# Kernel tuning notes

Hardware: AMD Instinct MI355X
Metric: run time of the kernel (lower is better)

## Reference

```python
import jax, jax.numpy as jnp
import numpy as np

N = 50000   # nodes
F = 128     # num_features (per branch)
E = 800000  # edges
G = 16      # graphs in batch
T = 3       # blocks per branch


def setup_inputs() -> dict:
    key = jax.random.key(0)
    ks = jax.random.split(key, 32)
    s = 0.05
    d = {}
    d["x"] = jax.random.normal(ks[0], (N, 2 * F), jnp.float32)
    d["edge_index"] = jax.random.randint(ks[1], (2, E), 0, N)
    d["edge_weight"] = jax.random.uniform(ks[2], (E,), jnp.float32)
    d["batch"] = jnp.sort(jax.random.randint(ks[3], (N,), 0, G))
    d["states"] = jax.random.randint(ks[4], (N,), 0, 2).astype(jnp.float32)

    def w(k, shape):
        return jax.random.normal(k, shape, jnp.float32) * s

    for i, p in enumerate(["p1", "p2"]):
        b = 5 + i * 5
        d[f"{p}_a0"] = w(ks[b], (T,))            # alpha0: Linear(1,1,bias=False) weight per block
        d[f"{p}_a1W"] = w(ks[b + 1], (T, F, F))    # alpha1 weight
        d[f"{p}_a1b"] = w(ks[b + 2], (T, F))       # alpha1 bias
        d[f"{p}_linW"] = w(ks[b + 3], (T, F, F))   # conv.lin weight
        d[f"{p}_linb"] = w(ks[b + 4], (T, F))      # conv.lin bias
    d["beta0_W"] = w(ks[15], (F, F))
    d["beta1_W"] = w(ks[16], (F, F))
    d["beta2_W"] = w(ks[17], (F, 2 * F))
    d["beta2_b"] = w(ks[18], (F,))
    d["gamma0_W"] = w(ks[19], (F, F))
    d["gamma1_W"] = w(ks[20], (F, F))
    d["gamma2_W"] = w(ks[21], (F, F))
    d["gamma3_W"] = w(ks[22], (3 * F // 2, 3 * F))
    d["gamma4_W"] = w(ks[23], (1, 3 * F // 2))
    d["gamma4_b"] = w(ks[24], (1,))
    return d


def _lrelu(v):
    return jax.nn.leaky_relu(v, 0.2)


def _block(x, states, a0, a1W, a1b, linW, linb, src, dst, ew):
    # x = lrelu(alpha1(x + alpha0(states)))
    h = _lrelu((x + states[:, None] * a0) @ a1W.T + a1b)
    # CustomGCNConv: lin then edge-weighted gather/scatter-add (source->target)
    h = h @ linW.T + linb
    msg = ew[:, None] * h[src]  # [E, F]
    return jax.ops.segment_sum(msg, dst, num_segments=x.shape[0])


def reference(x, edge_index, edge_weight, batch, states,
              p1_a0, p1_a1W, p1_a1b, p1_linW, p1_linb,
              p2_a0, p2_a1W, p2_a1b, p2_linW, p2_linb,
              beta0_W, beta1_W, beta2_W, beta2_b,
              gamma0_W, gamma1_W, gamma2_W, gamma3_W, gamma4_W, gamma4_b):
    Fh = x.shape[1] // 2
    x1, x2 = x[:, :Fh], x[:, Fh:]
    s0, s1 = edge_index[0], edge_index[1]
    x1s = jnp.zeros_like(x1)
    x2s = jnp.zeros_like(x2)
    for t in range(T):
        # branch1 uses reversed edges edge_index[[1,0]]
        x1 = _lrelu(_block(x1, states, p1_a0[t], p1_a1W[t], p1_a1b[t],
                           p1_linW[t], p1_linb[t], s1, s0, edge_weight))
        x2 = _lrelu(_block(x2, states, p2_a0[t], p2_a1W[t], p2_a1b[t],
                           p2_linW[t], p2_linb[t], s0, s1, edge_weight))
        x1s = x1s + x1
        x2s = x2s + x2
    xc = _lrelu(jnp.concatenate([x1s @ beta0_W.T, x2s @ beta1_W.T], -1) @ beta2_W.T + beta2_b)
    sel = (states == 1.0)[:, None]
    # per-graph pooled sums broadcast back to nodes (== repeat_interleave since batch is sorted)
    x_s = jax.ops.segment_sum(jnp.where(sel, xc, 0.0), batch, num_segments=G)[batch]
    x_sum = jax.ops.segment_sum(xc, batch, num_segments=G)[batch]
    h = jnp.concatenate([xc @ gamma0_W.T, x_s @ gamma1_W.T, x_sum @ gamma2_W.T], -1)
    h = _lrelu(h @ gamma3_W.T)
    return (h @ gamma4_W.T + gamma4_b).reshape(-1)
```

## Files before the change

### kernel.cpp

```cpp
#include <hip/hip_runtime.h>

typedef short s8v __attribute__((ext_vector_type(8)));
typedef float f32x4 __attribute__((ext_vector_type(4)));

#define LRELU(v) ((v) > 0.f ? (v) : 0.2f * (v))

constexpr int NBK = 391;
constexpr int TILE = 2048;
constexpr int CAP = 4096;

__device__ __forceinline__ float b2f(unsigned short b) {
  return __uint_as_float(((unsigned int)b) << 16);
}
__device__ __forceinline__ unsigned short f2b(float f) {
  unsigned int x = __float_as_uint(f);
  x += 0x7fffu + ((x >> 16) & 1u);
  return (unsigned short)(x >> 16);
}
__device__ __forceinline__ unsigned int pack2(float lo, float hi) {
  return ((unsigned int)f2b(hi) << 16) | (unsigned int)f2b(lo);
}

struct FArgs {
  const unsigned short* X[2];
  const unsigned short* W1[2];
  const float* b1[2];
  const float* a0p[2];
  const float* rowsum[2];
  const unsigned short* W2[2];
  const float* b2[2];
  unsigned short* H[2];
  const float* states;
  int N;
};

__global__ __launch_bounds__(256) void fused_mlp_kernel(FArgs fa)
{
  __shared__ __align__(16) unsigned short Ws[128 * 128];
  __shared__ __align__(16) unsigned short Tp[128 * 128];
  const int d = blockIdx.y;
  const int tid = threadIdx.x;
  const int lane = tid & 63;
  const int w = tid >> 6;
  const int l15 = lane & 15;
  const int g = lane >> 4;
  const int m0 = blockIdx.x * 128;
  const int N = fa.N;

#pragma unroll
  for (int j = 0; j < 8; ++j) {
    int idx = tid + j * 256;
    int o = idx >> 4, c = idx & 15;
    uint4 v = *(const uint4*)(fa.W1[d] + (size_t)o * 128 + c * 8);
    *(uint4*)&Ws[o * 128 + (c ^ (o & 15)) * 8] = v;
  }
  s8v a[2][4];
#pragma unroll
  for (int mf = 0; mf < 2; ++mf) {
    int row = m0 + w * 32 + mf * 16 + l15;
    const unsigned short* ar = fa.X[d] + (size_t)row * 128 + g * 8;
#pragma unroll
    for (int ks = 0; ks < 4; ++ks) {
      s8v t = {};
      if (row < N) t = *(const s8v*)(ar + ks * 32);
      a[mf][ks] = t;
    }
  }
  f32x4 zero4 = {0.f, 0.f, 0.f, 0.f};
  f32x4 acc[2][8];
#pragma unroll
  for (int mf = 0; mf < 2; ++mf)
#pragma unroll
    for (int nf = 0; nf < 8; ++nf) acc[mf][nf] = zero4;
  __syncthreads();
#pragma unroll
  for (int ks = 0; ks < 4; ++ks) {
#pragma unroll
    for (int nf = 0; nf < 8; ++nf) {
      int c = ks * 4 + g;
      s8v b = *(const s8v*)&Ws[(nf * 16 + l15) * 128 + (c ^ l15) * 8];
      acc[0][nf] = __builtin_amdgcn_mfma_f32_16x16x32_bf16(a[0][ks], b, acc[0][nf], 0, 0, 0);
      acc[1][nf] = __builtin_amdgcn_mfma_f32_16x16x32_bf16(a[1][ks], b, acc[1][nf], 0, 0, 0);
    }
  }
  const float a0 = fa.a0p[d][0];
#pragma unroll
  for (int mf = 0; mf < 2; ++mf) {
#pragma unroll
    for (int r = 0; r < 4; ++r) {
      int lrow = w * 32 + mf * 16 + g * 4 + r;
      int row = m0 + lrow;
      float sa = (row < N) ? fa.states[row] * a0 : 0.f;
#pragma unroll
      for (int nf = 0; nf < 8; ++nf) {
        int col = nf * 16 + l15;
        float v = 0.f;
        if (row < N) {
          v = acc[mf][nf][r] + fa.b1[d][col] + sa * fa.rowsum[d][col];
          v = LRELU(v);
        }
        int cch = col >> 3;
        Tp[lrow * 128 + ((cch ^ (lrow & 15)) << 3) + (col & 7)] = f2b(v);
      }
    }
  }
  __syncthreads();
#pragma unroll
  for (int j = 0; j < 8; ++j) {
    int idx = tid + j * 256;
    int o = idx >> 4, c = idx & 15;
    uint4 v = *(const uint4*)(fa.W2[d] + (size_t)o * 128 + c * 8);
    *(uint4*)&Ws[o * 128 + (c ^ (o & 15)) * 8] = v;
  }
  __syncthreads();
#pragma unroll
  for (int mf = 0; mf < 2; ++mf) {
    int lrow = w * 32 + mf * 16 + l15;
#pragma unroll
    for (int ks = 0; ks < 4; ++ks) {
      int c2 = ks * 4 + g;
      a[mf][ks] = *(const s8v*)&Tp[lrow * 128 + ((c2 ^ (lrow & 15)) << 3)];
    }
  }
#pragma unroll
  for (int mf = 0; mf < 2; ++mf)
#pragma unroll
    for (int nf = 0; nf < 8; ++nf) acc[mf][nf] = zero4;
#pragma unroll
  for (int ks = 0; ks < 4; ++ks) {
#pragma unroll
    for (int nf = 0; nf < 8; ++nf) {
      int c = ks * 4 + g;
      s8v b = *(const s8v*)&Ws[(nf * 16 + l15) * 128 + (c ^ l15) * 8];
      acc[0][nf] = __builtin_amdgcn_mfma_f32_16x16x32_bf16(a[0][ks], b, acc[0][nf], 0, 0, 0);
      acc[1][nf] = __builtin_amdgcn_mfma_f32_16x16x32_bf16(a[1][ks], b, acc[1][nf], 0, 0, 0);
    }
  }
#pragma unroll
  for (int mf = 0; mf < 2; ++mf) {
#pragma unroll
    for (int r = 0; r < 4; ++r) {
      int row = m0 + w * 32 + mf * 16 + g * 4 + r;
      if (row >= N) continue;
      unsigned short* crow = fa.H[d] + (size_t)row * 128;
#pragma unroll
      for (int nf = 0; nf < 8; ++nf) {
        int col = nf * 16 + l15;
        crow[col] = f2b(acc[mf][nf][r] + fa.b2[d][col]);
      }
    }
  }
}

struct PBArgs {
  const unsigned short* U[2];
  const unsigned short* Wb[2];
  const unsigned short* Wb2;
  const float* bias;
  unsigned short* XC;
  int N;
};

__global__ __launch_bounds__(256) void fused_beta_kernel(PBArgs pa)
{
  __shared__ __align__(16) unsigned short Ws[128 * 128];
  __shared__ __align__(16) unsigned short Tp[128 * 128];
  const int tid = threadIdx.x;
  const int lane = tid & 63;
  const int w = tid >> 6;
  const int l15 = lane & 15;
  const int g = lane >> 4;
  const int m0 = blockIdx.x * 128;
  const int N = pa.N;
  f32x4 zero4 = {0.f, 0.f, 0.f, 0.f};
  s8v a[2][4];
  f32x4 accf[2][8];
#pragma unroll
  for (int mf = 0; mf < 2; ++mf)
#pragma unroll
    for (int nf = 0; nf < 8; ++nf) accf[mf][nf] = zero4;

  for (int ph = 0; ph < 2; ++ph) {
#pragma unroll
    for (int j = 0; j < 8; ++j) {
      int idx = tid + j * 256;
      int o = idx >> 4, c = idx & 15;
      uint4 v = *(const uint4*)(pa.Wb[ph] + (size_t)o * 128 + c * 8);
      *(uint4*)&Ws[o * 128 + (c ^ (o & 15)) * 8] = v;
    }
#pragma unroll
    for (int mf = 0; mf < 2; ++mf) {
      int row = m0 + w * 32 + mf * 16 + l15;
      const unsigned short* ar = pa.U[ph] + (size_t)row * 128 + g * 8;
#pragma unroll
      for (int ks = 0; ks < 4; ++ks) {
        s8v t = {};
        if (row < N) t = *(const s8v*)(ar + ks * 32);
        a[mf][ks] = t;
      }
    }
    f32x4 acc[2][8];
#pragma unroll
    for (int mf = 0; mf < 2; ++mf)
#pragma unroll
      for (int nf = 0; nf < 8; ++nf) acc[mf][nf] = zero4;
    __syncthreads();
#pragma unroll
    for (int ks = 0; ks < 4; ++ks) {
#pragma unroll
      for (int nf = 0; nf < 8; ++nf) {
        int c = ks * 4 + g;
        s8v b = *(const s8v*)&Ws[(nf * 16 + l15) * 128 + (c ^ l15) * 8];
        acc[0][nf] = __builtin_amdgcn_mfma_f32_16x16x32_bf16(a[0][ks], b, acc[0][nf], 0, 0, 0);
        acc[1][nf] = __builtin_amdgcn_mfma_f32_16x16x32_bf16(a[1][ks], b, acc[1][nf], 0, 0, 0);
      }
    }
    __syncthreads();
#pragma unroll
    for (int mf = 0; mf < 2; ++mf) {
#pragma unroll
      for (int r = 0; r < 4; ++r) {
        int lrow = w * 32 + mf * 16 + g * 4 + r;
        int row = m0 + lrow;
#pragma unroll
        for (int nf = 0; nf < 8; ++nf) {
          int col = nf * 16 + l15;
          float v = (row < N) ? acc[mf][nf][r] : 0.f;
          int cch = col >> 3;
          Tp[lrow * 128 + ((cch ^ (lrow & 15)) << 3) + (col & 7)] = f2b(v);
        }
      }
    }
    __syncthreads();
#pragma unroll
    for (int j = 0; j < 8; ++j) {
      int idx = tid + j * 256;
      int o = idx >> 4, c = idx & 15;
      uint4 v = *(const uint4*)(pa.Wb2 + (size_t)o * 256 + ph * 128 + c * 8);
      *(uint4*)&Ws[o * 128 + (c ^ (o & 15)) * 8] = v;
    }
#pragma unroll
    for (int mf = 0; mf < 2; ++mf) {
      int lrow = w * 32 + mf * 16 + l15;
#pragma unroll
      for (int ks = 0; ks < 4; ++ks) {
        int c2 = ks * 4 + g;
        a[mf][ks] = *(const s8v*)&Tp[lrow * 128 + ((c2 ^ (lrow & 15)) << 3)];
      }
    }
    __syncthreads();
#pragma unroll
    for (int ks = 0; ks < 4; ++ks) {
#pragma unroll
      for (int nf = 0; nf < 8; ++nf) {
        int c = ks * 4 + g;
        s8v b = *(const s8v*)&Ws[(nf * 16 + l15) * 128 + (c ^ l15) * 8];
        accf[0][nf] = __builtin_amdgcn_mfma_f32_16x16x32_bf16(a[0][ks], b, accf[0][nf], 0, 0, 0);
        accf[1][nf] = __builtin_amdgcn_mfma_f32_16x16x32_bf16(a[1][ks], b, accf[1][nf], 0, 0, 0);
      }
    }
    __syncthreads();
  }
#pragma unroll
  for (int mf = 0; mf < 2; ++mf) {
#pragma unroll
    for (int r = 0; r < 4; ++r) {
      int row = m0 + w * 32 + mf * 16 + g * 4 + r;
      if (row >= N) continue;
      unsigned short* crow = pa.XC + (size_t)row * 128;
#pragma unroll
      for (int nf = 0; nf < 8; ++nf) {
        int col = nf * 16 + l15;
        float v = accf[mf][nf][r] + pa.bias[col];
        crow[col] = f2b(LRELU(v));
      }
    }
  }
}

__global__ __launch_bounds__(256) void g3_kernel(
    const unsigned short* __restrict__ xc,
    const unsigned short* __restrict__ A16,
    const unsigned short* __restrict__ B16,
    const int* __restrict__ batch,
    const unsigned short* __restrict__ W0,
    const unsigned short* __restrict__ W3,
    const float* __restrict__ g4W,
    const float* __restrict__ g4b,
    float* __restrict__ out, int N)
{
  constexpr int NF = 12;
  __shared__ __align__(16) unsigned short Ws[192 * 128];
  __shared__ __align__(16) unsigned short Tp[128 * 128];
  const int tid = threadIdx.x;
  const int lane = tid & 63;
  const int w = tid >> 6;
  const int l15 = lane & 15;
  const int g = lane >> 4;
  const int m0 = blockIdx.x * 128;

  f32x4 zero4 = {0.f, 0.f, 0.f, 0.f};
  s8v a[2][4];

#pragma unroll
  for (int j = 0; j < 8; ++j) {
    int idx = tid + j * 256;
    int o = idx >> 4, c = idx & 15;
    uint4 v = *(const uint4*)(W0 + (size_t)o * 128 + c * 8);
    *(uint4*)&Ws[o * 128 + (c ^ (o & 15)) * 8] = v;
  }
#pragma unroll
  for (int mf = 0; mf < 2; ++mf) {
    int row = m0 + w * 32 + mf * 16 + l15;
    const unsigned short* ar = xc + (size_t)row * 128 + g * 8;
#pragma unroll
    for (int ks = 0; ks < 4; ++ks) {
      s8v t = {};
      if (row < N) t = *(const s8v*)(ar + ks * 32);
      a[mf][ks] = t;
    }
  }
  {
    f32x4 acc1[2][8];
#pragma unroll
    for (int mf = 0; mf < 2; ++mf)
#pragma unroll
      for (int nf = 0; nf < 8; ++nf) acc1[mf][nf] = zero4;
    __syncthreads();
#pragma unroll
    for (int ks = 0; ks < 4; ++ks) {
#pragma unroll
      for (int nf = 0; nf < 8; ++nf) {
        int c = ks * 4 + g;
        s8v b = *(const s8v*)&Ws[(nf * 16 + l15) * 128 + (c ^ l15) * 8];
        acc1[0][nf] = __builtin_amdgcn_mfma_f32_16x16x32_bf16(a[0][ks], b, acc1[0][nf], 0, 0, 0);
        acc1[1][nf] = __builtin_amdgcn_mfma_f32_16x16x32_bf16(a[1][ks], b, acc1[1][nf], 0, 0, 0);
      }
    }
#pragma unroll
    for (int mf = 0; mf < 2; ++mf) {
#pragma unroll
      for (int r = 0; r < 4; ++r) {
        int lrow = w * 32 + mf * 16 + g * 4 + r;
        int row = m0 + lrow;
#pragma unroll
        for (int nf = 0; nf < 8; ++nf) {
          int col = nf * 16 + l15;
          float v = (row < N) ? acc1[mf][nf][r] : 0.f;
          int cch = col >> 3;
          Tp[lrow * 128 + ((cch ^ (lrow & 15)) << 3) + (col & 7)] = f2b(v);
        }
      }
    }
  }
  __syncthreads();

  f32x4 acc[2][NF];
#pragma unroll
  for (int mf = 0; mf < 2; ++mf)
#pragma unroll
    for (int nf = 0; nf < NF; ++nf) acc[mf][nf] = zero4;

  int brow[2];
#pragma unroll
  for (int mf = 0; mf < 2; ++mf) {
    int row = m0 + w * 32 + mf * 16 + l15;
    brow[mf] = (row < N) ? batch[row] : 0;
  }

  for (int kk = 0; kk < 384; kk += 128) {
#pragma unroll
    for (int j = 0; j < NF; ++j) {
      int idx = tid + j * 256;
      int o = idx >> 4, c = idx & 15;
      uint4 v = *(const uint4*)(W3 + (size_t)o * 384 + kk + c * 8);
      *(uint4*)&Ws[o * 128 + (c ^ (o & 15)) * 8] = v;
    }
    if (kk == 0) {
#pragma unroll
      for (int mf = 0; mf < 2; ++mf) {
        int lrow = w * 32 + mf * 16 + l15;
#pragma unroll
        for (int ks = 0; ks < 4; ++ks) {
          int c2 = ks * 4 + g;
          a[mf][ks] = *(const s8v*)&Tp[lrow * 128 + ((c2 ^ (lrow & 15)) << 3)];
        }
      }
    } else {
#pragma unroll
      for (int mf = 0; mf < 2; ++mf) {
        int row = m0 + w * 32 + mf * 16 + l15;
        const unsigned short* ar = ((kk == 128) ? A16 : B16) + (size_t)brow[mf] * 128 + g * 8;
#pragma unroll
        for (int ks = 0; ks < 4; ++ks) {
          s8v t = {};
          if (row < N) t = *(const s8v*)(ar + ks * 32);
          a[mf][ks] = t;
        }
      }
    }
    __syncthreads();
#pragma unroll
    for (int ks = 0; ks < 4; ++ks) {
#pragma unroll
      for (int nf = 0; nf < NF; ++nf) {
        int c = ks * 4 + g;
        s8v b = *(const s8v*)&Ws[(nf * 16 + l15) * 128 + (c ^ l15) * 8];
        acc[0][nf] = __builtin_amdgcn_mfma_f32_16x16x32_bf16(a[0][ks], b, acc[0][nf], 0, 0, 0);
        acc[1][nf] = __builtin_amdgcn_mfma_f32_16x16x32_bf16(a[1][ks], b, acc[1][nf], 0, 0, 0);
      }
    }
    if (kk < 256) __syncthreads();
  }

  float w4[NF];
#pragma unroll
  for (int nf = 0; nf < NF; ++nf) w4[nf] = g4W[nf * 16 + l15];
  const float gb = g4b[0];

#pragma unroll
  for (int mf = 0; mf < 2; ++mf) {
#pragma unroll
    for (int r = 0; r < 4; ++r) {
      int row = m0 + w * 32 + mf * 16 + g * 4 + r;
      float dot = 0.f;
#pragma unroll
      for (int nf = 0; nf < NF; ++nf) {
        float v = acc[mf][nf][r];
        v = LRELU(v);
        dot += v * w4[nf];
      }
#pragma unroll
      for (int m = 1; m < 16; m <<= 1) dot += __shfl_xor(dot, m, 16);
      if (l15 == 0 && row < N) out[row] = dot + gb;
    }
  }
}

struct PreArgs {
  const float* src[9];
  unsigned short* wreg;
  int cum[10];
  const float* a1; const float* a2; float* rs;
  const float* x;
  unsigned short* x1; unsigned short* x2;
  int* bcur0; int* bcur1;
  int n;
};

__global__ __launch_bounds__(256) void preamble_kernel(PreArgs pa)
{
  const int NINIT = 3125;
  const int NCONV = 172;
  int b = blockIdx.x;
  int t = threadIdx.x;
  if (b < NINIT) {
    int idx = b * 256 + t;
    if (idx < pa.n * 16) {
      int r = idx >> 4, c = idx & 15;
      const float* xr = pa.x + (size_t)r * 256 + c * 8;
      float4 p0 = *(const float4*)xr;
      float4 p1 = *(const float4*)(xr + 4);
      uint4 u1;
      u1.x = pack2(p0.x, p0.y); u1.y = pack2(p0.z, p0.w);
      u1.z = pack2(p1.x, p1.y); u1.w = pack2(p1.z, p1.w);
      float4 q0 = *(const float4*)(xr + 128);
      float4 q1 = *(const float4*)(xr + 132);
      uint4 u2;
      u2.x = pack2(q0.x, q0.y); u2.y = pack2(q0.z, q0.w);
      u2.z = pack2(q1.x, q1.y); u2.w = pack2(q1.z, q1.w);
      ((uint4*)(pa.x1 + (size_t)r * 128))[c] = u1;
      ((uint4*)(pa.x2 + (size_t)r * 128))[c] = u2;
    }
  } else if (b < NINIT + NCONV) {
    int e = ((b - NINIT) * 256 + t) * 8;
    if (e < pa.cum[9]) {
      int j = 0;
#pragma unroll
      for (int k = 1; k < 9; ++k) if (e >= pa.cum[k]) j = k;
      const float* s = pa.src[j] + (e - pa.cum[j]);
      float4 p0 = *(const float4*)s;
      float4 p1 = *(const float4*)(s + 4);
      uint4 u;
      u.x = pack2(p0.x, p0.y); u.y = pack2(p0.z, p0.w);
      u.z = pack2(p1.x, p1.y); u.w = pack2(p1.z, p1.w);
      *(uint4*)(pa.wreg + e) = u;
    }
  } else if (b < NINIT + NCONV + 6) {
    int j = b - NINIT - NCONV;
    if (t < 128) {
      const float* src = (j < 3) ? (pa.a1 + (size_t)j * 16384) : (pa.a2 + (size_t)(j - 3) * 16384);
      float s = 0.f;
      for (int k = 0; k < 128; ++k) s += src[t * 128 + k];
      pa.rs[j * 128 + t] = s;
    }
  } else {
    for (int i = t; i < NBK; i += 256) { pa.bcur0[i] = 0; pa.bcur1[i] = 0; }
  }
}

struct BinArgs {
  const int* s0; const int* s1; const float* ew;
  int* bcur0; int* bcur1;
  unsigned long long* bin0; unsigned long long* bin1;
  int E;
};
__global__ __launch_bounds__(256) void bin_kernel(BinArgs ba)
{
  __shared__ int hist0[NBK], hist1[NBK];
  __shared__ int base0[NBK], base1[NBK];
  const int t = threadIdx.x;
  const int e0 = blockIdx.x * TILE;
  const int e1 = min(e0 + TILE, ba.E);
  for (int i = t; i < NBK; i += 256) { hist0[i] = 0; hist1[i] = 0; }
  __syncthreads();
  for (int e = e0 + t; e < e1; e += 256) {
    atomicAdd(&hist0[ba.s0[e] >> 7], 1);
    atomicAdd(&hist1[ba.s1[e] >> 7], 1);
  }
  __syncthreads();
  for (int i = t; i < NBK; i += 256) {
    int c0 = hist0[i];
    base0[i] = c0 ? atomicAdd(&ba.bcur0[i], c0) : 0;
    int c1 = hist1[i];
    base1[i] = c1 ? atomicAdd(&ba.bcur1[i], c1) : 0;
  }
  __syncthreads();
  for (int i = t; i < NBK; i += 256) { hist0[i] = 0; hist1[i] = 0; }
  __syncthreads();
  for (int e = e0 + t; e < e1; e += 256) {
    int d0 = ba.s0[e], d1 = ba.s1[e];
    unsigned long long wb = (unsigned long long)__float_as_uint(ba.ew[e]) << 32;
    int b0 = d0 >> 7, b1 = d1 >> 7;
    int r0 = base0[b0] + atomicAdd(&hist0[b0], 1);
    if (r0 < CAP)
      ba.bin0[(size_t)b0 * CAP + r0] = wb | (unsigned int)((d0 & 127) << 16) | (unsigned int)d1;
    int r1 = base1[b1] + atomicAdd(&hist1[b1], 1);
    if (r1 < CAP)
      ba.bin1[(size_t)b1 * CAP + r1] = wb | (unsigned int)((d1 & 127) << 16) | (unsigned int)d0;
  }
}

struct BScanArgs { const int* cnt[2]; int* bbase[2]; float* gsel; float* gsum; };
__global__ __launch_bounds__(128) void bscan_kernel(BScanArgs a)
{
  __shared__ int ld[2][NBK];
  int wid = threadIdx.x >> 6, lane = threadIdx.x & 63;
  for (int i = threadIdx.x; i < 2048; i += 128) { a.gsel[i] = 0.f; a.gsum[i] = 0.f; }
  for (int i = lane; i < NBK; i += 64) ld[wid][i] = a.cnt[wid][i];
  __syncthreads();
  if (lane == 0) {
    int acc = 0;
    for (int i = 0; i < NBK; ++i) { int v = ld[wid][i]; ld[wid][i] = acc; acc += v; }
    a.bbase[wid][NBK] = acc;
  }
  __syncthreads();
  for (int i = lane; i < NBK; i += 64) a.bbase[wid][i] = ld[wid][i];
}

struct RArgs {
  const int* bbase[2];
  const unsigned long long* bin[2];
  unsigned int* comb[2];
  int* row[2];
  int n;
};
__global__ __launch_bounds__(256) void reorder_kernel(RArgs ra)
{
  const int d = blockIdx.y;
  const int b = blockIdx.x;
  const unsigned long long* __restrict__ bin = ra.bin[d] + (size_t)b * CAP;
  unsigned int* __restrict__ comb = ra.comb[d];
  int* __restrict__ row = ra.row[d];
  const int nb = b * 128;
  const int ne = min(nb + 128, ra.n);
  const int t = threadIdx.x;
  __shared__ int lcnt[128];
  __shared__ int lcur[128];
  __shared__ int wtot[4];
  if (t < 128) lcnt[t] = 0;
  const int span_beg = ra.bbase[d][b];
  const int span_end = ra.bbase[d][b + 1];
  const int cnt = span_end - span_beg;
  __syncthreads();
  for (int i = t; i < cnt; i += 256) {
    int nl = ((unsigned int)bin[i] >> 16) & 127;
    atomicAdd(&lcnt[nl], 1);
  }
  __syncthreads();
  int lane = t & 63, wv = t >> 6;
  int v = (t < 128) ? lcnt[t] : 0;
  int sc = v;
#pragma unroll
  for (int off = 1; off < 64; off <<= 1) {
    int u = __shfl_up(sc, off, 64);
    if (lane >= off) sc += u;
  }
  if (lane == 63) wtot[wv] = sc;
  __syncthreads();
  int excl = sc - v + ((wv == 1) ? wtot[0] : 0);
  if (t < 128) {
    lcur[t] = excl;
    if (nb + t < ne) row[nb + t] = span_beg + excl;
  }
  if (b == NBK - 1 && t == 0) row[ra.n] = span_end;
  __syncthreads();
  for (int i = t; i < cnt; i += 256) {
    unsigned long long r = bin[i];
    unsigned int lo = (unsigned int)r;
    float w = __uint_as_float((unsigned int)(r >> 32));
    int nl = (lo >> 16) & 127;
    int slot = atomicAdd(&lcur[nl], 1);
    comb[span_beg + slot] = (lo & 0xffffu) | ((unsigned int)f2b(w) << 16);
  }
}

struct GArgs {
  const int* rowstart[2];
  const unsigned int* comb[2];
  const unsigned short* h[2];
  unsigned short* xout[2];
  const unsigned int* add1[2];
  const unsigned int* add2[2];
  int n;
};
__global__ void gather_kernel(GArgs ga)
{
  int quad = blockIdx.x * (blockDim.x >> 6) + (threadIdx.x >> 6);
  int lane = threadIdx.x & 63;
  int sub = lane >> 4;
  int fl = lane & 15;
  long long gnode = (long long)4 * quad + sub;
  bool valid = gnode < 2 * ga.n;
  int dir = (valid && gnode >= ga.n) ? 1 : 0;
  int node = valid ? (int)(gnode - (long long)dir * ga.n) : 0;
  const int* __restrict__ rowstart = ga.rowstart[dir];
  const unsigned int* __restrict__ comb = ga.comb[dir];
  const unsigned int* __restrict__ h = (const unsigned int*)ga.h[dir];
  int beg = rowstart[node], end = rowstart[node + 1];
  if (!valid) end = beg;
  int nch_own = (end - beg + 7) >> 3;
  int m1 = max(nch_own, __shfl_xor(nch_own, 16, 64));
  int nch = max(m1, __shfl_xor(m1, 32, 64));
  float a0 = 0.f, a1 = 0.f, a2 = 0.f, a3 = 0.f;
  float a4 = 0.f, a5 = 0.f, a6 = 0.f, a7 = 0.f;
  for (int ch = 0; ch < nch; ++ch) {
    int p0 = beg + ch * 8;
    unsigned int cc[8];
    uint4 uu[8];
#pragma unroll
    for (int i = 0; i < 8; ++i) {
      int pi = p0 + i;
      cc[i] = (pi < end) ? comb[pi] : 0u;
    }
#pragma unroll
    for (int i = 0; i < 8; ++i)
      uu[i] = *(const uint4*)(h + (size_t)(cc[i] & 0xffffu) * 64 + fl * 4);
#pragma unroll
    for (int i = 0; i < 8; ++i) {
      float wv = b2f((unsigned short)(cc[i] >> 16));
      a0 += wv * b2f((unsigned short)uu[i].x);
      a1 += wv * b2f((unsigned short)(uu[i].x >> 16));
      a2 += wv * b2f((unsigned short)uu[i].y);
      a3 += wv * b2f((unsigned short)(uu[i].y >> 16));
      a4 += wv * b2f((unsigned short)uu[i].z);
      a5 += wv * b2f((unsigned short)(uu[i].z >> 16));
      a6 += wv * b2f((unsigned short)uu[i].w);
      a7 += wv * b2f((unsigned short)(uu[i].w >> 16));
    }
  }
  float v0 = LRELU(a0), v1 = LRELU(a1), v2 = LRELU(a2), v3 = LRELU(a3);
  float v4 = LRELU(a4), v5 = LRELU(a5), v6 = LRELU(a6), v7 = LRELU(a7);
  if (ga.add1[0]) {
    uint4 ua = ((const uint4*)ga.add1[dir])[(size_t)node * 16 + fl];
    uint4 ub = ((const uint4*)ga.add2[dir])[(size_t)node * 16 + fl];
    v0 += b2f((unsigned short)ua.x) + b2f((unsigned short)ub.x);
    v1 += b2f((unsigned short)(ua.x >> 16)) + b2f((unsigned short)(ub.x >> 16));
    v2 += b2f((unsigned short)ua.y) + b2f((unsigned short)ub.y);
    v3 += b2f((unsigned short)(ua.y >> 16)) + b2f((unsigned short)(ub.y >> 16));
    v4 += b2f((unsigned short)ua.z) + b2f((unsigned short)ub.z);
    v5 += b2f((unsigned short)(ua.z >> 16)) + b2f((unsigned short)(ub.z >> 16));
    v6 += b2f((unsigned short)ua.w) + b2f((unsigned short)ub.w);
    v7 += b2f((unsigned short)(ua.w >> 16)) + b2f((unsigned short)(ub.w >> 16));
  }
  if (valid) {
    uint4 o;
    o.x = pack2(v0, v1);
    o.y = pack2(v2, v3);
    o.z = pack2(v4, v5);
    o.w = pack2(v6, v7);
    ((uint4*)(ga.xout[dir] + (size_t)node * 128))[fl] = o;
  }
}

__global__ __launch_bounds__(256) void segsum_kernel(
    const unsigned short* __restrict__ xc, const int* __restrict__ batch,
    const float* __restrict__ states,
    float* __restrict__ gsel, float* __restrict__ gsum, int n)
{
  int slot = threadIdx.x >> 6;
  int lane = threadIdx.x & 63;
  int r0 = blockIdx.x * 128 + slot * 32;
  if (r0 >= n) return;
  int r1 = min(r0 + 32, n);
  const unsigned int* __restrict__ xcu = (const unsigned int*)xc;
  float sel0 = 0.f, sel1 = 0.f, sum0 = 0.f, sum1 = 0.f;
  int cur = batch[r0];
  for (int r = r0; r < r1; r += 4) {
    unsigned int u[4]; int bb[4]; float st[4];
#pragma unroll
    for (int i = 0; i < 4; ++i) {
      int ri = min(r + i, r1 - 1);
      u[i] = xcu[(size_t)ri * 64 + lane];
      bb[i] = batch[ri];
      st[i] = states[ri];
    }
    int m = min(4, r1 - r);
#pragma unroll
    for (int i = 0; i < 4; ++i) {
      if (i >= m) break;
      if (bb[i] != cur) {
        atomicAdd(&gsel[cur * 128 + lane * 2], sel0);
        atomicAdd(&gsel[cur * 128 + lane * 2 + 1], sel1);
        atomicAdd(&gsum[cur * 128 + lane * 2], sum0);
        atomicAdd(&gsum[cur * 128 + lane * 2 + 1], sum1);
        sel0 = sel1 = sum0 = sum1 = 0.f;
        cur = bb[i];
      }
      float lo = b2f((unsigned short)u[i]);
      float hi = b2f((unsigned short)(u[i] >> 16));
      sum0 += lo; sum1 += hi;
      if (st[i] == 1.0f) { sel0 += lo; sel1 += hi; }
    }
  }
  atomicAdd(&gsel[cur * 128 + lane * 2], sel0);
  atomicAdd(&gsel[cur * 128 + lane * 2 + 1], sel1);
  atomicAdd(&gsum[cur * 128 + lane * 2], sum0);
  atomicAdd(&gsum[cur * 128 + lane * 2 + 1], sum1);
}

__global__ void small16_kernel(const float* __restrict__ gsel, const float* __restrict__ gsum,
                               const float* __restrict__ g1W, const float* __restrict__ g2W,
                               unsigned short* __restrict__ A16, unsigned short* __restrict__ B16)
{
  int r = blockIdx.x, t = threadIdx.x, o = t & 127;
  const float* src = (t < 128) ? gsel : gsum;
  const float* Wm  = (t < 128) ? g1W : g2W;
  float acc = 0.f;
  for (int k = 0; k < 128; ++k) acc += src[r * 128 + k] * Wm[o * 128 + k];
  unsigned short* dst = (t < 128) ? A16 : B16;
  dst[r * 128 + o] = f2b(acc);
}

extern "C" void kernel_launch(void* const* d_in, const int* in_sizes, int n_in,
                              void* d_out, int out_size, void* d_ws, size_t ws_size,
                              hipStream_t stream)
{
  const int N = 50000, F = 128, E = 800000, G = 16, T = 3;
  const float* x      = (const float*)d_in[0];
  const int*   ei     = (const int*)d_in[1];
  const int*   s0     = ei;
  const int*   s1     = ei + E;
  const float* ew     = (const float*)d_in[2];
  const int*   batch  = (const int*)d_in[3];
  const float* states = (const float*)d_in[4];
  const float* p_a0[2]   = {(const float*)d_in[5],  (const float*)d_in[10]};
  const float* p_a1W[2]  = {(const float*)d_in[6],  (const float*)d_in[11]};
  const float* p_a1b[2]  = {(const float*)d_in[7],  (const float*)d_in[12]};
  const float* p_linW[2] = {(const float*)d_in[8],  (const float*)d_in[13]};
  const float* p_linb[2] = {(const float*)d_in[9],  (const float*)d_in[14]};
  const float* beta0W = (const float*)d_in[15];
  const float* beta1W = (const float*)d_in[16];
  const float* beta2W = (const float*)d_in[17];
  const float* beta2b = (const float*)d_in[18];
  const float* g0W = (const float*)d_in[19];
  const float* g1W = (const float*)d_in[20];
  const float* g2W = (const float*)d_in[21];
  const float* g3W = (const float*)d_in[22];
  const float* g4W = (const float*)d_in[23];
  const float* g4b = (const float*)d_in[24];
  float* out = (float*)d_out;

  char* p = (char*)d_ws;
  auto alloc = [&](size_t bytes) {
    char* r = p;
    p += (bytes + 255) & ~(size_t)255;
    return r;
  };
  const size_t NFb2 = (size_t)N * F * sizeof(unsigned short);
  unsigned short* X1[3] = {(unsigned short*)alloc(NFb2), (unsigned short*)alloc(NFb2),
                           (unsigned short*)alloc(NFb2)};
  unsigned short* X2[3] = {(unsigned short*)alloc(NFb2), (unsigned short*)alloc(NFb2),
                           (unsigned short*)alloc(NFb2)};
  unsigned short* TMP0 = (unsigned short*)alloc(NFb2);
  unsigned short* TMP1 = (unsigned short*)alloc(NFb2);
  unsigned short* HH0  = (unsigned short*)alloc(NFb2);
  unsigned short* HH1  = (unsigned short*)alloc(NFb2);
  int*   row0 = (int*)alloc((size_t)(N + 1) * 4);
  int*   row1 = (int*)alloc((size_t)(N + 1) * 4);
  int*   bbase0 = (int*)alloc((size_t)(NBK + 1) * 4);
  int*   bbase1 = (int*)alloc((size_t)(NBK + 1) * 4);
  int*   bcur0 = (int*)alloc((size_t)NBK * 4);
  int*   bcur1 = (int*)alloc((size_t)NBK * 4);
  unsigned long long* bin0 = (unsigned long long*)alloc((size_t)NBK * CAP * 8);
  unsigned long long* bin1 = (unsigned long long*)alloc((size_t)NBK * CAP * 8);
  unsigned int* comb0 = (unsigned int*)alloc((size_t)E * 4);
  unsigned int* comb1 = (unsigned int*)alloc((size_t)E * 4);
  float* gsel = (float*)alloc((size_t)G * F * 4);
  float* gsum = (float*)alloc((size_t)G * F * 4);
  unsigned short* A16b = (unsigned short*)alloc((size_t)G * F * 2);
  unsigned short* B16b = (unsigned short*)alloc((size_t)G * F * 2);
  unsigned short* wreg = (unsigned short*)alloc((size_t)352256 * 2);
  float* rs = (float*)alloc((size_t)6 * 128 * 4);

  unsigned short* a1Wb[2]  = {wreg + 0,      wreg + 49152};
  unsigned short* linWb[2] = {wreg + 98304,  wreg + 147456};
  unsigned short* b0b = wreg + 196608;
  unsigned short* b1b = wreg + 212992;
  unsigned short* b2b = wreg + 229376;
  unsigned short* g0b = wreg + 262144;
  unsigned short* g3b = wreg + 278528;

  const dim3 blk256(256);
  const int GX = (N + 127) / 128;
  const int EB = (E + TILE - 1) / TILE;

  PreArgs pra;
  pra.src[0] = p_a1W[0];  pra.src[1] = p_a1W[1];
  pra.src[2] = p_linW[0]; pra.src[3] = p_linW[1];
  pra.src[4] = beta0W;    pra.src[5] = beta1W;  pra.src[6] = beta2W;
  pra.src[7] = g0W;       pra.src[8] = g3W;
  pra.wreg = wreg;
  int cums[10] = {0, 49152, 98304, 147456, 196608, 212992, 229376, 262144, 278528, 352256};
  for (int i = 0; i < 10; ++i) pra.cum[i] = cums[i];
  pra.a1 = p_a1W[0]; pra.a2 = p_a1W[1]; pra.rs = rs;
  pra.x = x; pra.x1 = X1[0]; pra.x2 = X2[0];
  pra.bcur0 = bcur0; pra.bcur1 = bcur1;
  pra.n = N;
  preamble_kernel<<<3125 + 172 + 6 + 1, blk256, 0, stream>>>(pra);

  BinArgs bna;
  bna.s0 = s0; bna.s1 = s1; bna.ew = ew;
  bna.bcur0 = bcur0; bna.bcur1 = bcur1;
  bna.bin0 = bin0; bna.bin1 = bin1;
  bna.E = E;
  bin_kernel<<<EB, blk256, 0, stream>>>(bna);
  BScanArgs bsa;
  bsa.cnt[0] = bcur0; bsa.cnt[1] = bcur1;
  bsa.bbase[0] = bbase0; bsa.bbase[1] = bbase1;
  bsa.gsel = gsel; bsa.gsum = gsum;
  bscan_kernel<<<1, 128, 0, stream>>>(bsa);
  RArgs ra;
  ra.bbase[0] = bbase0; ra.bbase[1] = bbase1;
  ra.bin[0] = bin0; ra.bin[1] = bin1;
  ra.comb[0] = comb0; ra.comb[1] = comb1;
  ra.row[0] = row0; ra.row[1] = row1;
  ra.n = N;
  reorder_kernel<<<dim3(NBK, 2), blk256, 0, stream>>>(ra);

  for (int t = 0; t < T; ++t) {
    int rv = t % 3, wv = (t + 1) % 3;

    FArgs fa;
    fa.X[0] = X1[rv];  fa.X[1] = X2[rv];
    fa.W1[0] = a1Wb[0] + t * 16384;  fa.W1[1] = a1Wb[1] + t * 16384;
    fa.b1[0] = p_a1b[0] + t * F;     fa.b1[1] = p_a1b[1] + t * F;
    fa.a0p[0] = p_a0[0] + t;         fa.a0p[1] = p_a0[1] + t;
    fa.rowsum[0] = rs + t * 128;     fa.rowsum[1] = rs + (3 + t) * 128;
    fa.W2[0] = linWb[0] + t * 16384; fa.W2[1] = linWb[1] + t * 16384;
    fa.b2[0] = p_linb[0] + t * F;    fa.b2[1] = p_linb[1] + t * F;
    fa.H[0] = HH0;  fa.H[1] = HH1;
    fa.states = states;  fa.N = N;
    fused_mlp_kernel<<<dim3(GX, 2), blk256, 0, stream>>>(fa);

    GArgs ga;
    ga.rowstart[0] = row0; ga.rowstart[1] = row1;
    ga.comb[0] = comb0;    ga.comb[1] = comb1;
    ga.h[0] = HH0;         ga.h[1] = HH1;
    if (t == T - 1) {
      ga.xout[0] = TMP0;  ga.xout[1] = TMP1;
      ga.add1[0] = (const unsigned int*)X1[1];  ga.add1[1] = (const unsigned int*)X2[1];
      ga.add2[0] = (const unsigned int*)X1[2];  ga.add2[1] = (const unsigned int*)X2[2];
    } else {
      ga.xout[0] = X1[wv];  ga.xout[1] = X2[wv];
      ga.add1[0] = nullptr; ga.add1[1] = nullptr;
      ga.add2[0] = nullptr; ga.add2[1] = nullptr;
    }
    ga.n = N;
    gather_kernel<<<(2 * N + 15) / 16, blk256, 0, stream>>>(ga);
  }

  PBArgs pb;
  pb.U[0] = TMP0; pb.U[1] = TMP1;
  pb.Wb[0] = b0b; pb.Wb[1] = b1b; pb.Wb2 = b2b;
  pb.bias = beta2b; pb.XC = HH0; pb.N = N;
  fused_beta_kernel<<<GX, blk256, 0, stream>>>(pb);

  segsum_kernel<<<GX, blk256, 0, stream>>>(HH0, batch, states, gsel, gsum, N);
  small16_kernel<<<G, blk256, 0, stream>>>(gsel, gsum, g1W, g2W, A16b, B16b);

  g3_kernel<<<GX, blk256, 0, stream>>>(HH0, A16b, B16b, batch, g0b, g3b, g4W, g4b, out, N);
}
```

Before: 406.1 us.

## Sort gather nodes by degree to balance wavefront loop trip counts

Builds a per-direction degree histogram during reordering, then a new kernel produces a permutation grouping nodes by in-degree (capped at 63). The gather kernel processes nodes in this permuted order, so the four nodes sharing a wavefront have similar chunk counts and less divergence from the max-reduced loop bound. This adds a small kernel, atomics and an extra indirection, and scatters the output writes and row reads across memory.

```diff
diff --git a/kernel.cpp b/kernel.cpp
--- a/kernel.cpp
+++ b/kernel.cpp
@@ -541,12 +541,14 @@
   }
 }
 
-struct BScanArgs { const int* cnt[2]; int* bbase[2]; float* gsel; float* gsum; };
+struct BScanArgs { const int* cnt[2]; int* bbase[2]; float* gsel; float* gsum;
+                   int* dhist; int* dcur; };
 __global__ __launch_bounds__(128) void bscan_kernel(BScanArgs a)
 {
   __shared__ int ld[2][NBK];
   int wid = threadIdx.x >> 6, lane = threadIdx.x & 63;
   for (int i = threadIdx.x; i < 2048; i += 128) { a.gsel[i] = 0.f; a.gsum[i] = 0.f; }
+  if (threadIdx.x < 128) { a.dhist[threadIdx.x] = 0; a.dcur[threadIdx.x] = 0; }
   for (int i = lane; i < NBK; i += 64) ld[wid][i] = a.cnt[wid][i];
   __syncthreads();
   if (lane == 0) {
@@ -563,6 +565,7 @@
   const unsigned long long* bin[2];
   unsigned int* comb[2];
   int* row[2];
+  int* dhist;
   int n;
 };
 __global__ __launch_bounds__(256) void reorder_kernel(RArgs ra)
@@ -590,6 +593,7 @@
   __syncthreads();
   int lane = t & 63, wv = t >> 6;
   int v = (t < 128) ? lcnt[t] : 0;
+  if (t < 128 && nb + t < ne) atomicAdd(&ra.dhist[d * 64 + min(v, 63)], 1);
   int sc = v;
 #pragma unroll
   for (int off = 1; off < 64; off <<= 1) {
@@ -615,6 +619,31 @@
   }
 }
 
+struct DPArgs {
+  const int* row[2];
+  const int* dhist;
+  int* dcur;
+  int* perm[2];
+  int n;
+};
+__global__ __launch_bounds__(256) void dperm_kernel(DPArgs a)
+{
+  const int d = blockIdx.y;
+  const int i = blockIdx.x * 256 + threadIdx.x;
+  __shared__ int sbase[64];
+  if (threadIdx.x == 0) {
+    int acc = 0;
+    for (int k = 0; k < 64; ++k) { sbase[k] = acc; acc += a.dhist[d * 64 + k]; }
+  }
+  __syncthreads();
+  if (i < a.n) {
+    int deg = a.row[d][i + 1] - a.row[d][i];
+    int bin = min(deg, 63);
+    int pos = sbase[bin] + atomicAdd(&a.dcur[d * 64 + bin], 1);
+    a.perm[d][pos] = i;
+  }
+}
+
 struct GArgs {
   const int* rowstart[2];
   const unsigned int* comb[2];
@@ -622,6 +651,7 @@
   unsigned short* xout[2];
   const unsigned int* add1[2];
   const unsigned int* add2[2];
+  const int* perm[2];
   int n;
 };
 __global__ void gather_kernel(GArgs ga)
@@ -633,7 +663,8 @@
   long long gnode = (long long)4 * quad + sub;
   bool valid = gnode < 2 * ga.n;
   int dir = (valid && gnode >= ga.n) ? 1 : 0;
-  int node = valid ? (int)(gnode - (long long)dir * ga.n) : 0;
+  int pidx = valid ? (int)(gnode - (long long)dir * ga.n) : 0;
+  int node = ga.perm[dir][pidx];
   const int* __restrict__ rowstart = ga.rowstart[dir];
   const unsigned int* __restrict__ comb = ga.comb[dir];
   const unsigned int* __restrict__ h = (const unsigned int*)ga.h[dir];
@@ -806,6 +837,10 @@
   unsigned long long* bin1 = (unsigned long long*)alloc((size_t)NBK * CAP * 8);
   unsigned int* comb0 = (unsigned int*)alloc((size_t)E * 4);
   unsigned int* comb1 = (unsigned int*)alloc((size_t)E * 4);
+  int*   perm0 = (int*)alloc((size_t)N * 4);
+  int*   perm1 = (int*)alloc((size_t)N * 4);
+  int*   dhist = (int*)alloc((size_t)128 * 4);
+  int*   dcur  = (int*)alloc((size_t)128 * 4);
   float* gsel = (float*)alloc((size_t)G * F * 4);
   float* gsum = (float*)alloc((size_t)G * F * 4);
   unsigned short* A16b = (unsigned short*)alloc((size_t)G * F * 2);
@@ -849,14 +884,22 @@
   bsa.cnt[0] = bcur0; bsa.cnt[1] = bcur1;
   bsa.bbase[0] = bbase0; bsa.bbase[1] = bbase1;
   bsa.gsel = gsel; bsa.gsum = gsum;
+  bsa.dhist = dhist; bsa.dcur = dcur;
   bscan_kernel<<<1, 128, 0, stream>>>(bsa);
   RArgs ra;
   ra.bbase[0] = bbase0; ra.bbase[1] = bbase1;
   ra.bin[0] = bin0; ra.bin[1] = bin1;
   ra.comb[0] = comb0; ra.comb[1] = comb1;
   ra.row[0] = row0; ra.row[1] = row1;
+  ra.dhist = dhist;
   ra.n = N;
   reorder_kernel<<<dim3(NBK, 2), blk256, 0, stream>>>(ra);
+  DPArgs dpa;
+  dpa.row[0] = row0; dpa.row[1] = row1;
+  dpa.dhist = dhist; dpa.dcur = dcur;
+  dpa.perm[0] = perm0; dpa.perm[1] = perm1;
+  dpa.n = N;
+  dperm_kernel<<<dim3((N + 255) / 256, 2), blk256, 0, stream>>>(dpa);
 
   for (int t = 0; t < T; ++t) {
     int rv = t % 3, wv = (t + 1) % 3;
@@ -877,6 +920,7 @@
     ga.rowstart[0] = row0; ga.rowstart[1] = row1;
     ga.comb[0] = comb0;    ga.comb[1] = comb1;
     ga.h[0] = HH0;         ga.h[1] = HH1;
+    ga.perm[0] = perm0;    ga.perm[1] = perm1;
     if (t == T - 1) {
       ga.xout[0] = TMP0;  ga.xout[1] = TMP1;
       ga.add1[0] = (const unsigned int*)X1[1];  ga.add1[1] = (const unsigned int*)X2[1];
```

New measurement: 690.9 us. +70.1%, slower.

## Sort nodes by in-degree before gather to balance wavefront work

Applied to the files above, without the earlier changes.

Builds a degree histogram per node block in the reorder kernel, scans it in a new dscan kernel, and scatters node ids into a degree-sorted permutation in a new dscat kernel. The gather kernel then handles nodes in that permuted order, so the four nodes sharing a wavefront have similar edge counts and the chunk-loop maximum wastes fewer iterations. The cost is two extra small kernel launches plus an indirect perm lookup, and neighbouring outputs are no longer written to contiguous rows.

```diff
diff --git a/kernel.cpp b/kernel.cpp
--- a/kernel.cpp
+++ b/kernel.cpp
@@ -563,6 +563,7 @@
   const unsigned long long* bin[2];
   unsigned int* comb[2];
   int* row[2];
+  int* dcnt;
   int n;
 };
 __global__ __launch_bounds__(256) void reorder_kernel(RArgs ra)
@@ -578,7 +579,9 @@
   __shared__ int lcnt[128];
   __shared__ int lcur[128];
   __shared__ int wtot[4];
+  __shared__ int h64[64];
   if (t < 128) lcnt[t] = 0;
+  if (t >= 128 && t < 192) h64[t - 128] = 0;
   const int span_beg = ra.bbase[d][b];
   const int span_end = ra.bbase[d][b + 1];
   const int cnt = span_end - span_beg;
@@ -590,6 +593,7 @@
   __syncthreads();
   int lane = t & 63, wv = t >> 6;
   int v = (t < 128) ? lcnt[t] : 0;
+  if (t < 128 && nb + t < ne) atomicAdd(&h64[min(v, 63)], 1);
   int sc = v;
 #pragma unroll
   for (int off = 1; off < 64; off <<= 1) {
@@ -604,6 +608,7 @@
     if (nb + t < ne) row[nb + t] = span_beg + excl;
   }
   if (b == NBK - 1 && t == 0) row[ra.n] = span_end;
+  if (t < 64) ra.dcnt[((size_t)d * 64 + t) * NBK + b] = h64[t];
   __syncthreads();
   for (int i = t; i < cnt; i += 256) {
     unsigned long long r = bin[i];
@@ -615,6 +620,48 @@
   }
 }
 
+__global__ __launch_bounds__(128) void dscan_kernel(int* __restrict__ dcnt)
+{
+  int tid = threadIdx.x;
+  __shared__ int btot[128];
+  __shared__ int bbase[128];
+  int* rowp = dcnt + (size_t)tid * NBK;
+  int acc = 0;
+  for (int b = 0; b < NBK; ++b) { int c = rowp[b]; rowp[b] = acc; acc += c; }
+  btot[tid] = acc;
+  __syncthreads();
+  if (tid < 2) {
+    int a2 = 0;
+    for (int k = 0; k < 64; ++k) { bbase[tid * 64 + k] = a2; a2 += btot[tid * 64 + k]; }
+  }
+  __syncthreads();
+  int off = bbase[tid];
+  for (int b = 0; b < NBK; ++b) rowp[b] += off;
+}
+
+struct DSArgs {
+  const int* row[2];
+  const int* dcnt;
+  int* perm[2];
+  int n;
+};
+__global__ __launch_bounds__(256) void dscat_kernel(DSArgs a)
+{
+  const int d = blockIdx.y;
+  const int b = blockIdx.x;
+  const int t = threadIdx.x;
+  __shared__ int scur[64];
+  if (t < 64) scur[t] = a.dcnt[((size_t)d * 64 + t) * NBK + b];
+  __syncthreads();
+  int node = b * 128 + t;
+  if (t < 128 && node < a.n) {
+    int deg = a.row[d][node + 1] - a.row[d][node];
+    int bin = min(deg, 63);
+    int pos = atomicAdd(&scur[bin], 1);
+    a.perm[d][pos] = node;
+  }
+}
+
 struct GArgs {
   const int* rowstart[2];
   const unsigned int* comb[2];
@@ -622,6 +669,7 @@
   unsigned short* xout[2];
   const unsigned int* add1[2];
   const unsigned int* add2[2];
+  const int* perm[2];
   int n;
 };
 __global__ void gather_kernel(GArgs ga)
@@ -633,10 +681,12 @@
   long long gnode = (long long)4 * quad + sub;
   bool valid = gnode < 2 * ga.n;
   int dir = (valid && gnode >= ga.n) ? 1 : 0;
-  int node = valid ? (int)(gnode - (long long)dir * ga.n) : 0;
+  int pidx = valid ? (int)(gnode - (long long)dir * ga.n) : 0;
+  int node = ga.perm[dir][pidx];
   const int* __restrict__ rowstart = ga.rowstart[dir];
   const unsigned int* __restrict__ comb = ga.comb[dir];
-  const unsigned int* __restrict__ h = (const unsigned int*)ga.h[dir];
+  const unsigned short* __restrict__ hh = ga.h[dir];
+  const unsigned int* __restrict__ h = (const unsigned int*)hh;
   int beg = rowstart[node], end = rowstart[node + 1];
   if (!valid) end = beg;
   int nch_own = (end - beg + 7) >> 3;
@@ -806,6 +856,9 @@
   unsigned long long* bin1 = (unsigned long long*)alloc((size_t)NBK * CAP * 8);
   unsigned int* comb0 = (unsigned int*)alloc((size_t)E * 4);
   unsigned int* comb1 = (unsigned int*)alloc((size_t)E * 4);
+  int*   perm0 = (int*)alloc((size_t)N * 4);
+  int*   perm1 = (int*)alloc((size_t)N * 4);
+  int*   dcnt  = (int*)alloc((size_t)2 * 64 * NBK * 4);
   float* gsel = (float*)alloc((size_t)G * F * 4);
   float* gsum = (float*)alloc((size_t)G * F * 4);
   unsigned short* A16b = (unsigned short*)alloc((size_t)G * F * 2);
@@ -855,8 +908,16 @@
   ra.bin[0] = bin0; ra.bin[1] = bin1;
   ra.comb[0] = comb0; ra.comb[1] = comb1;
   ra.row[0] = row0; ra.row[1] = row1;
+  ra.dcnt = dcnt;
   ra.n = N;
   reorder_kernel<<<dim3(NBK, 2), blk256, 0, stream>>>(ra);
+  dscan_kernel<<<1, 128, 0, stream>>>(dcnt);
+  DSArgs dsa;
+  dsa.row[0] = row0; dsa.row[1] = row1;
+  dsa.dcnt = dcnt;
+  dsa.perm[0] = perm0; dsa.perm[1] = perm1;
+  dsa.n = N;
+  dscat_kernel<<<dim3(NBK, 2), blk256, 0, stream>>>(dsa);
 
   for (int t = 0; t < T; ++t) {
     int rv = t % 3, wv = (t + 1) % 3;
@@ -877,6 +938,7 @@
     ga.rowstart[0] = row0; ga.rowstart[1] = row1;
     ga.comb[0] = comb0;    ga.comb[1] = comb1;
     ga.h[0] = HH0;         ga.h[1] = HH1;
+    ga.perm[0] = perm0;    ga.perm[1] = perm1;
     if (t == T - 1) {
       ga.xout[0] = TMP0;  ga.xout[1] = TMP1;
       ga.add1[0] = (const unsigned int*)X1[1];  ga.add1[1] = (const unsigned int*)X2[1];
```

Result: slower. 447.3 us (+10.1%).
